# Optimization experiments

Hardware: AMD Instinct MI355X
Metric: run time of the kernel (lower is better)

Reference implementation:

```python
import jax, jax.numpy as jnp
import numpy as np

B, N, D, OUT = 8192, 256, 128, 10  # batch, input_dim (sites), bond_dim, output_dim
LOCAL = 2  # local physical dimension (hardcoded in source)


def setup_inputs() -> dict:
    key = jax.random.key(0)
    ks = jax.random.split(key, 6)
    scale = 1.0 / np.sqrt(D)  # stable variant of source's 0.1 init (keeps 256-site product O(1))
    x = jax.random.normal(ks[0], (B, N), dtype=jnp.float32)
    first = jax.random.normal(ks[1], (1, LOCAL, D), dtype=jnp.float32) * scale   # site 0: (1,2,D)
    mid = jax.random.normal(ks[2], (N - 2, D, LOCAL, D), dtype=jnp.float32) * scale  # sites 1..N-2
    last = jax.random.normal(ks[3], (D, LOCAL, 1), dtype=jnp.float32) * scale    # site N-1: (D,2,1)
    w = jax.random.normal(ks[4], (OUT, 1), dtype=jnp.float32) * 0.1  # nn.Linear(1, OUT) weight
    b = jnp.zeros((OUT,), dtype=jnp.float32)                          # nn.Linear(1, OUT) bias
    return {"x": x, "first": first, "mid": mid, "last": last, "w": w, "b": b}


def _feature_map(x):
    # per-sample min/max normalization over the feature axis, then (cos, sin) embedding
    x_min = jnp.min(x, axis=1, keepdims=True)
    x_max = jnp.max(x, axis=1, keepdims=True)
    x_norm = (x - x_min) / (x_max - x_min + 1e-6)
    ang = (np.pi / 2) * x_norm
    return jnp.stack([jnp.cos(ang), jnp.sin(ang)], axis=2)  # [B, N, 2]


def reference(x, first, mid, last, w, b):
    phi = _feature_map(x)  # [B, N, 2]
    # site 0: left[b, r] = sum_d first[0, d, r] * phi[b, 0, d]
    left = jnp.einsum('dr,bd->br', first[0], phi[:, 0])  # [B, D]
    # sites 1..N-2 via scan: left <- sum_{l,d} left[b,l] * M[l,d,r] * phi[b,i,d]
    phi_mid = jnp.swapaxes(phi[:, 1:-1], 0, 1)  # [N-2, B, 2]

    def step(left, inputs):
        M, p = inputs  # M: [D, 2, D], p: [B, 2]
        left = jnp.einsum('bl,ldr,bd->br', left, M, p)
        return left, None

    left, _ = jax.lax.scan(step, left, (mid, phi_mid))  # [B, D]
    # last site: scalar[b] = sum_{l,d} left[b,l] * last[l,d,0] * phi[b,N-1,d]
    scalar = jnp.einsum('bl,ld,bd->b', left, last[:, :, 0], phi[:, -1])  # [B]
    # nn.Linear(1, OUT): logits = scalar * w^T + b
    logits = scalar[:, None] * w[:, 0][None, :] + b  # [B, OUT]
    return logits
```

## Files before the change

### kernel.cpp

```cpp
#include <hip/hip_runtime.h>


typedef _Float16 v8h __attribute__((ext_vector_type(8)));
typedef _Float16 h2  __attribute__((ext_vector_type(2)));
typedef float    v4f __attribute__((ext_vector_type(4)));

#define PI_HALF 1.5707963267948966f
#define SITE_U4 4096

union U4H8 { uint4 u; v8h h; };

__device__ __forceinline__ v4f mfma16h(uint4 a, uint4 b, v4f c){
  U4H8 ua, ub; ua.u = a; ub.u = b;
  return __builtin_amdgcn_mfma_f32_16x16x32_f16(ua.h, ub.h, c, 0, 0, 0);
}
__device__ __forceinline__ unsigned pack2h(float lo, float hi){
  h2 p; p[0] = (_Float16)lo; p[1] = (_Float16)hi;
  return __builtin_bit_cast(unsigned, p);
}

__global__ __launch_bounds__(256) void repack_mid(const float* __restrict__ mid,
                                                  unsigned short* __restrict__ wsB){
  int idx  = blockIdx.x * 256 + threadIdx.x;
  int lg   = idx & 15;
  int nt   = (idx >> 4) & 7;
  int kt   = (idx >> 7) & 3;
  int d    = (idx >> 9) & 1;
  int site = idx >> 10;
  int q    = lg >> 2;
  int n0   = 16*nt + 4*(lg & 3);
  const float* src = mid + ((size_t)(site*128 + 32*kt + 8*q)*2 + d)*128 + n0;
  float V[8][4];
  #pragma unroll
  for (int j = 0; j < 8; ++j){
    float4 a = *(const float4*)(src + (size_t)j*256);
    V[j][0]=a.x; V[j][1]=a.y; V[j][2]=a.z; V[j][3]=a.w;
  }
  uint4* dst = (uint4*)wsB + ((((size_t)site*2 + d)*4 + kt)*8 + nt)*64
             + 16*q + 4*(lg & 3);
  #pragma unroll
  for (int t = 0; t < 4; ++t){
    uint4 o;
    o.x = pack2h(V[0][t], V[1][t]);
    o.y = pack2h(V[2][t], V[3][t]);
    o.z = pack2h(V[4][t], V[5][t]);
    o.w = pack2h(V[6][t], V[7][t]);
    dst[t] = o;
  }
}

__global__ __launch_bounds__(512, 2) void mps_main(
    const float* __restrict__ x,
    const float* __restrict__ first,
    const unsigned short* __restrict__ wsB,
    const float* __restrict__ lastw,
    const float* __restrict__ wlin,
    const float* __restrict__ blin,
    float* __restrict__ out)
{
  __shared__ unsigned phiT[256*36];
  __shared__ unsigned AfragU[2*2*4*64*4];
  __shared__ float scal[32];

  const int tid  = threadIdx.x;
  const int g    = blockIdx.x;
  const int w    = tid >> 6;
  const int lane = tid & 63;
  const int r    = lane & 15;
  const int q    = lane >> 4;
  const int rowbase = g * 32;
  const int physL = lane ^ ((lane >> 3) & 7);
  const int rh    = r >> 3;

  {
    const int row = tid >> 4;
    const int c0  = (tid & 15) * 16;
    const float4* xp = (const float4*)(x + (size_t)(rowbase + row) * 256 + c0);
    float xv[16];
    float vmin = 3.0e38f, vmax = -3.0e38f;
    #pragma unroll
    for (int c = 0; c < 4; ++c){
      float4 u = xp[c];
      xv[c*4+0] = u.x; xv[c*4+1] = u.y; xv[c*4+2] = u.z; xv[c*4+3] = u.w;
      vmin = fminf(vmin, fminf(fminf(u.x,u.y), fminf(u.z,u.w)));
      vmax = fmaxf(vmax, fmaxf(fmaxf(u.x,u.y), fmaxf(u.z,u.w)));
    }
    #pragma unroll
    for (int m = 1; m < 16; m <<= 1){
      vmin = fminf(vmin, __shfl_xor(vmin, m));
      vmax = fmaxf(vmax, __shfl_xor(vmax, m));
    }
    const float sc = PI_HALF / (vmax - vmin + 1e-6f);
    #pragma unroll
    for (int j = 0; j < 16; ++j){
      float a = (xv[j] - vmin) * sc;
      phiT[(c0 + j)*36 + row] = pack2h(__cosf(a), __sinf(a));
    }
  }
  __syncthreads();

  {
    const int mt = w >> 2, kt = w & 3;
    float f0[8], f1[8];
    #pragma unroll
    for (int j = 0; j < 8; ++j){
      int l = 32*kt + 8*q + j;
      f0[j] = first[l];
      f1[j] = first[128 + l];
    }
    h2 ph0 = __builtin_bit_cast(h2, phiT[0*36 + 16*mt + r]);
    const float c0 = (float)ph0[0], s0 = (float)ph0[1];
    uint4 o;
    o.x = pack2h(f0[0]*c0 + f1[0]*s0, f0[1]*c0 + f1[1]*s0);
    o.y = pack2h(f0[2]*c0 + f1[2]*s0, f0[3]*c0 + f1[3]*s0);
    o.z = pack2h(f0[4]*c0 + f1[4]*s0, f0[5]*c0 + f1[5]*s0);
    o.w = pack2h(f0[6]*c0 + f1[6]*s0, f0[7]*c0 + f1[7]*s0);
    *(uint4*)&AfragU[2048 + ((mt*4 + kt)*64 + physL)*4] = o;
  }

  uint4 Breg0[8], Breg1[8];
  {
    const uint4* bp = (const uint4*)wsB;
    #pragma unroll
    for (int d = 0; d < 2; ++d)
      #pragma unroll
      for (int kt = 0; kt < 4; ++kt)
        Breg0[d*4+kt] = bp[(size_t)((d*4 + kt)*8 + w)*64 + lane];
  }

  auto body = [&](int site, uint4 (&Bcur)[8], uint4 (&Bnxt)[8]){
    __syncthreads();

    {
      const int soff = (site <= 253) ? site : 0;
      const uint4* bp = (const uint4*)wsB + (size_t)soff * SITE_U4;
      #pragma unroll
      for (int d = 0; d < 2; ++d)
        #pragma unroll
        for (int kt = 0; kt < 4; ++kt)
          Bnxt[d*4+kt] = bp[(size_t)((d*4 + kt)*8 + w)*64 + lane];
    }

    v4f acc0[2] = {};
    v4f acc1[2] = {};
    const unsigned* Abuf = &AfragU[(site & 1) * 2048];
    #pragma unroll
    for (int kt = 0; kt < 4; ++kt){
      uint4 a0 = *(const uint4*)&Abuf[((0*4 + kt)*64 + physL)*4];
      uint4 a1 = *(const uint4*)&Abuf[((1*4 + kt)*64 + physL)*4];
      acc0[0] = mfma16h(a0, Bcur[0 + kt], acc0[0]);
      acc0[1] = mfma16h(a1, Bcur[0 + kt], acc0[1]);
      acc1[0] = mfma16h(a0, Bcur[4 + kt], acc1[0]);
      acc1[1] = mfma16h(a1, Bcur[4 + kt], acc1[1]);
    }

    if (site < 254){
      unsigned short* Wb = (unsigned short*)&AfragU[((site+1) & 1) * 2048];
      const int X = 4*(w & 1) + 2*rh + (q >> 1);
      const int S0 = 32*(w & 1) + 16*rh + 4*q;
      #pragma unroll
      for (int mt = 0; mt < 2; ++mt){
        uint4 phiu = *(const uint4*)&phiT[site*36 + 16*mt + 4*q];
        const unsigned pr[4] = {phiu.x, phiu.y, phiu.z, phiu.w};
        const int base16 = (mt*4 + (w >> 1))*512;
        #pragma unroll
        for (int reg = 0; reg < 4; ++reg){
          h2 ph = __builtin_bit_cast(h2, pr[reg]);
          float v = (float)ph[0]*acc0[mt][reg]
                  + (float)ph[1]*acc1[mt][reg];
          const int phys = (S0 + reg) ^ X;
          Wb[base16 + phys*8 + (r & 7)] =
              __builtin_bit_cast(unsigned short, (_Float16)v);
        }
      }
    } else {
      float pA[2][4] = {};
      float pB[2][4] = {};
      const int l = 16*w + r;
      float2 gg = *(const float2*)(lastw + 2*l);
      #pragma unroll
      for (int mt = 0; mt < 2; ++mt){
        uint4 p4 = *(const uint4*)&phiT[254*36 + 16*mt + 4*q];
        const unsigned pr4[4] = {p4.x, p4.y, p4.z, p4.w};
        #pragma unroll
        for (int reg = 0; reg < 4; ++reg){
          h2 ph = __builtin_bit_cast(h2, pr4[reg]);
          float v = (float)ph[0]*acc0[mt][reg]
                  + (float)ph[1]*acc1[mt][reg];
          pA[mt][reg] += v * gg.x;
          pB[mt][reg] += v * gg.y;
        }
      }
      float part[2][4];
      #pragma unroll
      for (int mt = 0; mt < 2; ++mt){
        uint4 p5 = *(const uint4*)&phiT[255*36 + 16*mt + 4*q];
        const unsigned pr5[4] = {p5.x, p5.y, p5.z, p5.w};
        #pragma unroll
        for (int reg = 0; reg < 4; ++reg){
          h2 ph = __builtin_bit_cast(h2, pr5[reg]);
          part[mt][reg] = (float)ph[0]*pA[mt][reg] + (float)ph[1]*pB[mt][reg];
        }
      }
      #pragma unroll
      for (int m = 1; m < 16; m <<= 1)
        #pragma unroll
        for (int mt = 0; mt < 2; ++mt)
          #pragma unroll
          for (int reg = 0; reg < 4; ++reg)
            part[mt][reg] += __shfl_xor(part[mt][reg], m);
      if (tid < 32) scal[tid] = 0.0f;
      __syncthreads();
      if (r == 0){
        #pragma unroll
        for (int mt = 0; mt < 2; ++mt)
          #pragma unroll
          for (int reg = 0; reg < 4; ++reg)
            atomicAdd(&scal[16*mt + 4*q + reg], part[mt][reg]);
      }
      __syncthreads();
      for (int t = tid; t < 320; t += 512){
        int bb = t / 10, o = t - bb*10;
        out[(size_t)(rowbase + bb)*10 + o] = scal[bb]*wlin[o] + blin[o];
      }
    }
  };

  #pragma unroll 1
  for (int i = 1; i <= 253; i += 2){
    body(i,     Breg0, Breg1);
    body(i + 1, Breg1, Breg0);
  }
}

extern "C" void kernel_launch(void* const* d_in, const int* in_sizes, int n_in,
                              void* d_out, int out_size, void* d_ws, size_t ws_size,
                              hipStream_t stream){
  (void)in_sizes; (void)n_in; (void)out_size; (void)ws_size;
  const float* x     = (const float*)d_in[0];
  const float* first = (const float*)d_in[1];
  const float* mid   = (const float*)d_in[2];
  const float* lastw = (const float*)d_in[3];
  const float* wlin  = (const float*)d_in[4];
  const float* blin  = (const float*)d_in[5];
  float* o            = (float*)d_out;
  unsigned short* wsB = (unsigned short*)d_ws;

  hipLaunchKernelGGL(repack_mid, dim3(1016), dim3(256), 0, stream, mid, wsB);
  hipLaunchKernelGGL(mps_main,   dim3(256),  dim3(512), 0, stream,
                     x, first, wsB, lastw, wlin, blin, o);
}
```

Baseline: 285.3 us.

## Contract MPS chain from both ends concurrently and meet in the middle

Splits the 254-site sequential chain into a left sweep (waves 0-3) and a right sweep (waves 4-7) that run at the same time. The serial dependency depth drops from 254 to 127 steps, and the two partial environments are joined with a dot product at the end. Each wave now issues twice as many MFMAs and holds twice as many B registers per step. The repack kernel also writes a second, transposed copy of mid for the right sweep. Risks include more register pressure, double the workspace traffic, and a changed fp16 rounding order.

Result: faster. 269.7 us (-5.5%).

```diff
diff --git a/kernel.cpp b/kernel.cpp
--- a/kernel.cpp
+++ b/kernel.cpp
@@ -7,6 +7,7 @@
 
 #define PI_HALF 1.5707963267948966f
 #define SITE_U4 4096
+#define TOFF_U4 (254*4096)
 
 union U4H8 { uint4 u; v8h h; };
 
@@ -21,56 +22,85 @@
 
 __global__ __launch_bounds__(256) void repack_mid(const float* __restrict__ mid,
                                                   unsigned short* __restrict__ wsB){
-  int idx  = blockIdx.x * 256 + threadIdx.x;
-  int lg   = idx & 15;
-  int nt   = (idx >> 4) & 7;
-  int kt   = (idx >> 7) & 3;
-  int d    = (idx >> 9) & 1;
-  int site = idx >> 10;
-  int q    = lg >> 2;
-  int n0   = 16*nt + 4*(lg & 3);
-  const float* src = mid + ((size_t)(site*128 + 32*kt + 8*q)*2 + d)*128 + n0;
-  float V[8][4];
-  #pragma unroll
-  for (int j = 0; j < 8; ++j){
-    float4 a = *(const float4*)(src + (size_t)j*256);
-    V[j][0]=a.x; V[j][1]=a.y; V[j][2]=a.z; V[j][3]=a.w;
-  }
-  uint4* dst = (uint4*)wsB + ((((size_t)site*2 + d)*4 + kt)*8 + nt)*64
-             + 16*q + 4*(lg & 3);
-  #pragma unroll
-  for (int t = 0; t < 4; ++t){
-    uint4 o;
-    o.x = pack2h(V[0][t], V[1][t]);
-    o.y = pack2h(V[2][t], V[3][t]);
-    o.z = pack2h(V[4][t], V[5][t]);
-    o.w = pack2h(V[6][t], V[7][t]);
-    dst[t] = o;
+  const int bid = blockIdx.x;
+  if (bid < 1016){
+    int idx  = bid * 256 + threadIdx.x;
+    int lg   = idx & 15;
+    int nt   = (idx >> 4) & 7;
+    int kt   = (idx >> 7) & 3;
+    int d    = (idx >> 9) & 1;
+    int site = idx >> 10;
+    int q    = lg >> 2;
+    int n0   = 16*nt + 4*(lg & 3);
+    const float* src = mid + ((size_t)(site*128 + 32*kt + 8*q)*2 + d)*128 + n0;
+    float V[8][4];
+    #pragma unroll
+    for (int j = 0; j < 8; ++j){
+      float4 a = *(const float4*)(src + (size_t)j*256);
+      V[j][0]=a.x; V[j][1]=a.y; V[j][2]=a.z; V[j][3]=a.w;
+    }
+    uint4* dst = (uint4*)wsB + ((((size_t)site*2 + d)*4 + kt)*8 + nt)*64
+               + 16*q + 4*(lg & 3);
+    #pragma unroll
+    for (int t = 0; t < 4; ++t){
+      uint4 o;
+      o.x = pack2h(V[0][t], V[1][t]);
+      o.y = pack2h(V[2][t], V[3][t]);
+      o.z = pack2h(V[4][t], V[5][t]);
+      o.w = pack2h(V[6][t], V[7][t]);
+      dst[t] = o;
+    }
+  } else {
+    int idx  = (bid - 1016) * 256 + threadIdx.x;
+    int lg   = idx & 15;
+    int kt   = (idx >> 4) & 3;
+    int am   = (idx >> 6) & 7;
+    int d    = (idx >> 9) & 1;
+    int site = idx >> 10;
+    int q    = lg >> 2;
+    int m0   = 16*am + 4*(lg & 3);
+    int k0   = 32*kt + 8*q;
+    uint4* dst = (uint4*)wsB + TOFF_U4
+               + ((((size_t)site*2 + d)*8 + am)*4 + kt)*64 + 16*q + 4*(lg & 3);
+    #pragma unroll
+    for (int mp = 0; mp < 4; ++mp){
+      const float* src = mid + ((size_t)((site*128 + m0 + mp)*2) + d)*128 + k0;
+      float4 a = *(const float4*)(src);
+      float4 b = *(const float4*)(src + 4);
+      uint4 o;
+      o.x = pack2h(a.x, a.y);
+      o.y = pack2h(a.z, a.w);
+      o.z = pack2h(b.x, b.y);
+      o.w = pack2h(b.z, b.w);
+      dst[mp] = o;
+    }
   }
 }
 
 __global__ __launch_bounds__(512, 2) void mps_main(
     const float* __restrict__ x,
     const float* __restrict__ first,
-    const unsigned short* __restrict__ wsB,
+    const unsigned short* __restrict__ wsBv,
     const float* __restrict__ lastw,
     const float* __restrict__ wlin,
     const float* __restrict__ blin,
     float* __restrict__ out)
 {
   __shared__ unsigned phiT[256*36];
-  __shared__ unsigned AfragU[2*2*4*64*4];
+  __shared__ unsigned Af[2*2*4*64*4];
+  __shared__ unsigned Rf[2*4*2*64*4];
+  __shared__ float Rcomb[128*33];
   __shared__ float scal[32];
 
   const int tid  = threadIdx.x;
-  const int g    = blockIdx.x;
+  const int gblk = blockIdx.x;
   const int w    = tid >> 6;
   const int lane = tid & 63;
   const int r    = lane & 15;
   const int q    = lane >> 4;
-  const int rowbase = g * 32;
+  const int rh   = r >> 3;
+  const int rowbase = gblk * 32;
   const int physL = lane ^ ((lane >> 3) & 7);
-  const int rh    = r >> 3;
 
   {
     const int row = tid >> 4;
@@ -99,138 +129,241 @@
   }
   __syncthreads();
 
-  {
-    const int mt = w >> 2, kt = w & 3;
-    float f0[8], f1[8];
-    #pragma unroll
-    for (int j = 0; j < 8; ++j){
-      int l = 32*kt + 8*q + j;
-      f0[j] = first[l];
-      f1[j] = first[128 + l];
-    }
-    h2 ph0 = __builtin_bit_cast(h2, phiT[0*36 + 16*mt + r]);
-    const float c0 = (float)ph0[0], s0 = (float)ph0[1];
-    uint4 o;
-    o.x = pack2h(f0[0]*c0 + f1[0]*s0, f0[1]*c0 + f1[1]*s0);
-    o.y = pack2h(f0[2]*c0 + f1[2]*s0, f0[3]*c0 + f1[3]*s0);
-    o.z = pack2h(f0[4]*c0 + f1[4]*s0, f0[5]*c0 + f1[5]*s0);
-    o.w = pack2h(f0[6]*c0 + f1[6]*s0, f0[7]*c0 + f1[7]*s0);
-    *(uint4*)&AfragU[2048 + ((mt*4 + kt)*64 + physL)*4] = o;
-  }
-
-  uint4 Breg0[8], Breg1[8];
-  {
-    const uint4* bp = (const uint4*)wsB;
+  uint4 B0[16], B1[16];
+  if (w < 4){
+    const uint4* bp = (const uint4*)wsBv;
     #pragma unroll
     for (int d = 0; d < 2; ++d)
       #pragma unroll
       for (int kt = 0; kt < 4; ++kt)
-        Breg0[d*4+kt] = bp[(size_t)((d*4 + kt)*8 + w)*64 + lane];
-  }
-
-  auto body = [&](int site, uint4 (&Bcur)[8], uint4 (&Bnxt)[8]){
+        #pragma unroll
+        for (int nb = 0; nb < 2; ++nb)
+          B0[(d*4+kt)*2+nb] = bp[(size_t)((d*4 + kt)*8 + 2*w + nb)*64 + lane];
+  } else {
+    const int ww = w - 4;
+    const uint4* bp = (const uint4*)wsBv + TOFF_U4 + (size_t)253 * SITE_U4;
+    #pragma unroll
+    for (int d = 0; d < 2; ++d)
+      #pragma unroll
+      for (int mtl = 0; mtl < 2; ++mtl)
+        #pragma unroll
+        for (int kt = 0; kt < 4; ++kt)
+          B0[(d*2+mtl)*4+kt] = bp[(size_t)((d*8 + 2*ww + mtl)*4 + kt)*64 + lane];
+  }
+
+  if (w < 4){
+    float f0[8], f1[8];
+    #pragma unroll
+    for (int j = 0; j < 8; ++j){
+      int l = 32*w + 8*q + j;
+      f0[j] = first[l]; f1[j] = first[128 + l];
+    }
+    #pragma unroll
+    for (int mt = 0; mt < 2; ++mt){
+      h2 ph0 = __builtin_bit_cast(h2, phiT[0*36 + 16*mt + r]);
+      const float c0 = (float)ph0[0], s0 = (float)ph0[1];
+      uint4 o;
+      o.x = pack2h(f0[0]*c0 + f1[0]*s0, f0[1]*c0 + f1[1]*s0);
+      o.y = pack2h(f0[2]*c0 + f1[2]*s0, f0[3]*c0 + f1[3]*s0);
+      o.z = pack2h(f0[4]*c0 + f1[4]*s0, f0[5]*c0 + f1[5]*s0);
+      o.w = pack2h(f0[6]*c0 + f1[6]*s0, f0[7]*c0 + f1[7]*s0);
+      *(uint4*)&Af[((mt*4 + w)*64 + physL)*4] = o;
+    }
+  } else {
+    const int ww = w - 4;
+    float g0[8], g1[8];
+    #pragma unroll
+    for (int j = 0; j < 8; ++j){
+      int rr = 32*ww + 8*q + j;
+      float2 gg = *(const float2*)(lastw + 2*rr);
+      g0[j] = gg.x; g1[j] = gg.y;
+    }
+    #pragma unroll
+    for (int nt = 0; nt < 2; ++nt){
+      h2 p5 = __builtin_bit_cast(h2, phiT[255*36 + 16*nt + r]);
+      const float cb = (float)p5[0], sb = (float)p5[1];
+      uint4 o;
+      o.x = pack2h(g0[0]*cb + g1[0]*sb, g0[1]*cb + g1[1]*sb);
+      o.y = pack2h(g0[2]*cb + g1[2]*sb, g0[3]*cb + g1[3]*sb);
+      o.z = pack2h(g0[4]*cb + g1[4]*sb, g0[5]*cb + g1[5]*sb);
+      o.w = pack2h(g0[6]*cb + g1[6]*sb, g0[7]*cb + g1[7]*sb);
+      *(uint4*)&Rf[((ww*2 + nt)*64 + physL)*4] = o;
+    }
+  }
+
+  auto body = [&](int t, uint4 (&Fc)[16], uint4 (&Fn)[16]){
     __syncthreads();
-
-    {
-      const int soff = (site <= 253) ? site : 0;
-      const uint4* bp = (const uint4*)wsB + (size_t)soff * SITE_U4;
+    float vf[2][2][4];
+
+    if (w < 4){
+      {
+        const int soff = (t < 126) ? (t + 1) : 0;
+        const uint4* bp = (const uint4*)wsBv + (size_t)soff * SITE_U4;
+        #pragma unroll
+        for (int d = 0; d < 2; ++d)
+          #pragma unroll
+          for (int kt = 0; kt < 4; ++kt)
+            #pragma unroll
+            for (int nb = 0; nb < 2; ++nb)
+              Fn[(d*4+kt)*2+nb] = bp[(size_t)((d*4 + kt)*8 + 2*w + nb)*64 + lane];
+      }
+      v4f ac0[2][2] = {};
+      v4f ac1[2][2] = {};
+      const unsigned* Ab = &Af[(t & 1) * 2048];
       #pragma unroll
-      for (int d = 0; d < 2; ++d)
-        #pragma unroll
-        for (int kt = 0; kt < 4; ++kt)
-          Bnxt[d*4+kt] = bp[(size_t)((d*4 + kt)*8 + w)*64 + lane];
-    }
-
-    v4f acc0[2] = {};
-    v4f acc1[2] = {};
-    const unsigned* Abuf = &AfragU[(site & 1) * 2048];
-    #pragma unroll
-    for (int kt = 0; kt < 4; ++kt){
-      uint4 a0 = *(const uint4*)&Abuf[((0*4 + kt)*64 + physL)*4];
-      uint4 a1 = *(const uint4*)&Abuf[((1*4 + kt)*64 + physL)*4];
-      acc0[0] = mfma16h(a0, Bcur[0 + kt], acc0[0]);
-      acc0[1] = mfma16h(a1, Bcur[0 + kt], acc0[1]);
-      acc1[0] = mfma16h(a0, Bcur[4 + kt], acc1[0]);
-      acc1[1] = mfma16h(a1, Bcur[4 + kt], acc1[1]);
-    }
-
-    if (site < 254){
-      unsigned short* Wb = (unsigned short*)&AfragU[((site+1) & 1) * 2048];
-      const int X = 4*(w & 1) + 2*rh + (q >> 1);
-      const int S0 = 32*(w & 1) + 16*rh + 4*q;
+      for (int kt = 0; kt < 4; ++kt){
+        uint4 a0 = *(const uint4*)&Ab[((0*4 + kt)*64 + physL)*4];
+        uint4 a1 = *(const uint4*)&Ab[((1*4 + kt)*64 + physL)*4];
+        #pragma unroll
+        for (int nb = 0; nb < 2; ++nb){
+          ac0[0][nb] = mfma16h(a0, Fc[(0*4+kt)*2+nb], ac0[0][nb]);
+          ac0[1][nb] = mfma16h(a1, Fc[(0*4+kt)*2+nb], ac0[1][nb]);
+          ac1[0][nb] = mfma16h(a0, Fc[(1*4+kt)*2+nb], ac1[0][nb]);
+          ac1[1][nb] = mfma16h(a1, Fc[(1*4+kt)*2+nb], ac1[1][nb]);
+        }
+      }
+      if (t < 126){
+        unsigned short* Wb = (unsigned short*)&Af[((t+1) & 1) * 2048];
+        #pragma unroll
+        for (int mt = 0; mt < 2; ++mt){
+          uint4 phiu = *(const uint4*)&phiT[(t+1)*36 + 16*mt + 4*q];
+          const unsigned pr[4] = {phiu.x, phiu.y, phiu.z, phiu.w};
+          #pragma unroll
+          for (int nb = 0; nb < 2; ++nb){
+            const int S0 = 32*nb + 16*rh + 4*q;
+            const int X  = 4*nb + 2*rh + (q >> 1);
+            #pragma unroll
+            for (int reg = 0; reg < 4; ++reg){
+              h2 ph = __builtin_bit_cast(h2, pr[reg]);
+              float v = (float)ph[0]*ac0[mt][nb][reg]
+                      + (float)ph[1]*ac1[mt][nb][reg];
+              Wb[((mt*4 + w)*64 + ((S0 + reg) ^ X))*8 + (r & 7)] =
+                  __builtin_bit_cast(unsigned short, (_Float16)v);
+            }
+          }
+        }
+      } else {
+        #pragma unroll
+        for (int mt = 0; mt < 2; ++mt){
+          uint4 phiu = *(const uint4*)&phiT[127*36 + 16*mt + 4*q];
+          const unsigned pr[4] = {phiu.x, phiu.y, phiu.z, phiu.w};
+          #pragma unroll
+          for (int nb = 0; nb < 2; ++nb)
+            #pragma unroll
+            for (int reg = 0; reg < 4; ++reg){
+              h2 ph = __builtin_bit_cast(h2, pr[reg]);
+              vf[mt][nb][reg] = (float)ph[0]*ac0[mt][nb][reg]
+                              + (float)ph[1]*ac1[mt][nb][reg];
+            }
+        }
+      }
+    } else {
+      const int ww = w - 4;
+      {
+        const int soff = (t < 126) ? (252 - t) : 253;
+        const uint4* bp = (const uint4*)wsBv + TOFF_U4 + (size_t)soff * SITE_U4;
+        #pragma unroll
+        for (int d = 0; d < 2; ++d)
+          #pragma unroll
+          for (int mtl = 0; mtl < 2; ++mtl)
+            #pragma unroll
+            for (int kt = 0; kt < 4; ++kt)
+              Fn[(d*2+mtl)*4+kt] = bp[(size_t)((d*8 + 2*ww + mtl)*4 + kt)*64 + lane];
+      }
+      v4f ac0[2][2] = {};
+      v4f ac1[2][2] = {};
+      const unsigned* Rb = &Rf[(t & 1) * 2048];
       #pragma unroll
-      for (int mt = 0; mt < 2; ++mt){
-        uint4 phiu = *(const uint4*)&phiT[site*36 + 16*mt + 4*q];
-        const unsigned pr[4] = {phiu.x, phiu.y, phiu.z, phiu.w};
-        const int base16 = (mt*4 + (w >> 1))*512;
-        #pragma unroll
-        for (int reg = 0; reg < 4; ++reg){
-          h2 ph = __builtin_bit_cast(h2, pr[reg]);
-          float v = (float)ph[0]*acc0[mt][reg]
-                  + (float)ph[1]*acc1[mt][reg];
-          const int phys = (S0 + reg) ^ X;
-          Wb[base16 + phys*8 + (r & 7)] =
-              __builtin_bit_cast(unsigned short, (_Float16)v);
-        }
-      }
-    } else {
-      float pA[2][4] = {};
-      float pB[2][4] = {};
-      const int l = 16*w + r;
-      float2 gg = *(const float2*)(lastw + 2*l);
-      #pragma unroll
-      for (int mt = 0; mt < 2; ++mt){
-        uint4 p4 = *(const uint4*)&phiT[254*36 + 16*mt + 4*q];
-        const unsigned pr4[4] = {p4.x, p4.y, p4.z, p4.w};
-        #pragma unroll
-        for (int reg = 0; reg < 4; ++reg){
-          h2 ph = __builtin_bit_cast(h2, pr4[reg]);
-          float v = (float)ph[0]*acc0[mt][reg]
-                  + (float)ph[1]*acc1[mt][reg];
-          pA[mt][reg] += v * gg.x;
-          pB[mt][reg] += v * gg.y;
-        }
-      }
-      float part[2][4];
-      #pragma unroll
-      for (int mt = 0; mt < 2; ++mt){
-        uint4 p5 = *(const uint4*)&phiT[255*36 + 16*mt + 4*q];
-        const unsigned pr5[4] = {p5.x, p5.y, p5.z, p5.w};
-        #pragma unroll
-        for (int reg = 0; reg < 4; ++reg){
-          h2 ph = __builtin_bit_cast(h2, pr5[reg]);
-          part[mt][reg] = (float)ph[0]*pA[mt][reg] + (float)ph[1]*pB[mt][reg];
-        }
-      }
-      #pragma unroll
-      for (int m = 1; m < 16; m <<= 1)
-        #pragma unroll
-        for (int mt = 0; mt < 2; ++mt)
-          #pragma unroll
-          for (int reg = 0; reg < 4; ++reg)
-            part[mt][reg] += __shfl_xor(part[mt][reg], m);
+      for (int kt = 0; kt < 4; ++kt){
+        uint4 b0 = *(const uint4*)&Rb[((kt*2 + 0)*64 + physL)*4];
+        uint4 b1 = *(const uint4*)&Rb[((kt*2 + 1)*64 + physL)*4];
+        #pragma unroll
+        for (int mtl = 0; mtl < 2; ++mtl){
+          ac0[mtl][0] = mfma16h(Fc[(0*2+mtl)*4+kt], b0, ac0[mtl][0]);
+          ac0[mtl][1] = mfma16h(Fc[(0*2+mtl)*4+kt], b1, ac0[mtl][1]);
+          ac1[mtl][0] = mfma16h(Fc[(1*2+mtl)*4+kt], b0, ac1[mtl][0]);
+          ac1[mtl][1] = mfma16h(Fc[(1*2+mtl)*4+kt], b1, ac1[mtl][1]);
+        }
+      }
+      const int ps = 254 - t;
+      if (t < 126){
+        unsigned short* Wr = (unsigned short*)&Rf[((t+1) & 1) * 2048];
+        #pragma unroll
+        for (int nb = 0; nb < 2; ++nb){
+          h2 ph = __builtin_bit_cast(h2, phiT[ps*36 + 16*nb + r]);
+          const float cb = (float)ph[0], sb = (float)ph[1];
+          #pragma unroll
+          for (int mtl = 0; mtl < 2; ++mtl){
+            const int S0 = 32*mtl + 16*(q >> 1) + r;
+            const int phys = S0 ^ ((S0 >> 3) & 7);
+            #pragma unroll
+            for (int reg = 0; reg < 4; ++reg){
+              float v = cb*ac0[mtl][nb][reg] + sb*ac1[mtl][nb][reg];
+              Wr[((ww*2 + nb)*64 + phys)*8 + ((4*q + reg) & 7)] =
+                  __builtin_bit_cast(unsigned short, (_Float16)v);
+            }
+          }
+        }
+      } else {
+        #pragma unroll
+        for (int nb = 0; nb < 2; ++nb){
+          h2 ph = __builtin_bit_cast(h2, phiT[ps*36 + 16*nb + r]);
+          const float cb = (float)ph[0], sb = (float)ph[1];
+          #pragma unroll
+          for (int mtl = 0; mtl < 2; ++mtl)
+            #pragma unroll
+            for (int reg = 0; reg < 4; ++reg){
+              float v = cb*ac0[mtl][nb][reg] + sb*ac1[mtl][nb][reg];
+              int l = 32*ww + 16*mtl + 4*q + reg;
+              Rcomb[l*33 + 16*nb + r] = v;
+            }
+        }
+      }
+    }
+
+    if (t == 126){
       if (tid < 32) scal[tid] = 0.0f;
       __syncthreads();
-      if (r == 0){
+      if (w < 4){
+        float p[2][4] = {};
         #pragma unroll
         for (int mt = 0; mt < 2; ++mt)
           #pragma unroll
-          for (int reg = 0; reg < 4; ++reg)
-            atomicAdd(&scal[16*mt + 4*q + reg], part[mt][reg]);
+          for (int nb = 0; nb < 2; ++nb){
+            const int l = 32*w + 16*nb + r;
+            #pragma unroll
+            for (int reg = 0; reg < 4; ++reg)
+              p[mt][reg] += vf[mt][nb][reg] * Rcomb[l*33 + 16*mt + 4*q + reg];
+          }
+        #pragma unroll
+        for (int m = 1; m < 16; m <<= 1)
+          #pragma unroll
+          for (int mt = 0; mt < 2; ++mt)
+            #pragma unroll
+            for (int reg = 0; reg < 4; ++reg)
+              p[mt][reg] += __shfl_xor(p[mt][reg], m);
+        if (r == 0){
+          #pragma unroll
+          for (int mt = 0; mt < 2; ++mt)
+            #pragma unroll
+            for (int reg = 0; reg < 4; ++reg)
+              atomicAdd(&scal[16*mt + 4*q + reg], p[mt][reg]);
+        }
       }
       __syncthreads();
-      for (int t = tid; t < 320; t += 512){
-        int bb = t / 10, o = t - bb*10;
+      for (int t2 = tid; t2 < 320; t2 += 512){
+        int bb = t2 / 10, o = t2 - bb*10;
         out[(size_t)(rowbase + bb)*10 + o] = scal[bb]*wlin[o] + blin[o];
       }
     }
   };
 
   #pragma unroll 1
-  for (int i = 1; i <= 253; i += 2){
-    body(i,     Breg0, Breg1);
-    body(i + 1, Breg1, Breg0);
-  }
+  for (int t = 0; t < 126; t += 2){
+    body(t,     B0, B1);
+    body(t + 1, B1, B0);
+  }
+  body(126, B0, B1);
 }
 
 extern "C" void kernel_launch(void* const* d_in, const int* in_sizes, int n_in,
@@ -246,7 +379,7 @@
   float* o            = (float*)d_out;
   unsigned short* wsB = (unsigned short*)d_ws;
 
-  hipLaunchKernelGGL(repack_mid, dim3(1016), dim3(256), 0, stream, mid, wsB);
+  hipLaunchKernelGGL(repack_mid, dim3(2032), dim3(256), 0, stream, mid, wsB);
   hipLaunchKernelGGL(mps_main,   dim3(256),  dim3(512), 0, stream,
                      x, first, wsB, lastw, wlin, blin, o);
 }
```
